# Kernel tuning notes

Measured on AMD Instinct MI355X. Metric: run time of the kernel, lower is better.

Reference implementation:

```python
import jax, jax.numpy as jnp
import numpy as np

D_MODEL = 1024
N_HEADS = 16
HEAD_DIM = D_MODEL // N_HEADS
ROPE_BASE = 10000.0


def _rope_cos_sin(seq_len, dtype):
    half = HEAD_DIM // 2
    theta = 1.0 / (ROPE_BASE ** (jnp.arange(half, dtype=jnp.float32) / half))
    freqs = jnp.arange(seq_len, dtype=jnp.float32)[:, None] * theta[None, :]  # [S, half]
    cos = jnp.repeat(jnp.cos(freqs), 2, axis=-1).astype(dtype)  # [S, HEAD_DIM]
    sin = jnp.repeat(jnp.sin(freqs), 2, axis=-1).astype(dtype)
    return cos[None, None, :, :], sin[None, None, :, :]


def _rotate_half(x):
    x_even = x[..., ::2]
    x_odd = x[..., 1::2]
    return jnp.stack((-x_odd, x_even), axis=-1).reshape(x.shape)


def setup_inputs() -> dict:
    key = jax.random.key(0)
    k1, k2, k3, k4, k5 = jax.random.split(key, 5)
    bsz, seq_len = 4, 2048
    s = 1.0 / np.sqrt(D_MODEL)
    return {
        "x": jax.random.normal(k1, (bsz, seq_len, D_MODEL), dtype=jnp.float32),
        "W_qkv": jax.random.uniform(k2, (3 * D_MODEL, D_MODEL), minval=-s, maxval=s, dtype=jnp.float32),
        "b_qkv": jax.random.uniform(k3, (3 * D_MODEL,), minval=-s, maxval=s, dtype=jnp.float32),
        "W_out": jax.random.uniform(k4, (D_MODEL, D_MODEL), minval=-s, maxval=s, dtype=jnp.float32),
        "b_out": jax.random.uniform(k5, (D_MODEL,), minval=-s, maxval=s, dtype=jnp.float32),
    }


def reference(x, W_qkv, b_qkv, W_out, b_out):
    bsz, seq_len, _ = x.shape
    qkv = x @ W_qkv.T + b_qkv  # [B, S, 3*D]
    qkv = qkv.reshape(bsz, seq_len, 3, N_HEADS, HEAD_DIM)
    q = jnp.transpose(qkv[:, :, 0], (0, 2, 1, 3))  # [B, H, S, Dh]
    k = jnp.transpose(qkv[:, :, 1], (0, 2, 1, 3))
    v = jnp.transpose(qkv[:, :, 2], (0, 2, 1, 3))
    cos, sin = _rope_cos_sin(seq_len, x.dtype)
    q = q * cos + _rotate_half(q) * sin
    k = k * cos + _rotate_half(k) * sin
    attn = jnp.einsum("bhqd,bhkd->bhqk", q, k) / jnp.sqrt(jnp.asarray(HEAD_DIM, x.dtype))
    attn = jax.nn.softmax(attn, axis=-1)
    out = jnp.einsum("bhqk,bhkd->bhqd", attn, v)  # [B, H, S, Dh]
    out = jnp.transpose(out, (0, 2, 1, 3)).reshape(bsz, seq_len, D_MODEL)
    return out @ W_out.T + b_out
```

## Files before the change

### kernel.cpp

```cpp
#include <hip/hip_runtime.h>
#include <math.h>

typedef unsigned int u32;
typedef unsigned short u16;
typedef short bf16x8 __attribute__((ext_vector_type(8)));
typedef u32 u32x4 __attribute__((ext_vector_type(4)));
typedef float f32x4 __attribute__((ext_vector_type(4)));

#define SEQ 2048
#define NH 16
#define HD 64
#define DM 1024

#define QSCALE 0.1803368801111204f

static __device__ __forceinline__ u16 f2bf(float f) {
  u32 u = __builtin_bit_cast(u32, f);
  u32 r = (u + 0x7FFFu + ((u >> 16) & 1u)) >> 16;
  return (u16)r;
}

#define GLDS16(gsrc, ldst)                                                        \
  __builtin_amdgcn_global_load_lds(                                               \
      (const __attribute__((address_space(1))) void*)(gsrc),                      \
      (__attribute__((address_space(3))) void*)(ldst), 16, 0, 0)

static __device__ __forceinline__ int swz64(int r, int c) {
  return (r * 64 + c) ^ ((r & 7) * 8);
}

static __device__ __forceinline__ void swz_grid(int nx, int& bx, int& by) {
  int lid = blockIdx.y * nx + blockIdx.x;
  int nwg = nx * (int)gridDim.y;
  int chunk = nwg >> 3;
  int s = (lid & 7) * chunk + (lid >> 3);
  bx = s % nx;
  by = s / nx;
}

__global__ void cast_bf16_kernel(const float* __restrict__ src, u16* __restrict__ dst, int n) {
  int i = (blockIdx.x * blockDim.x + threadIdx.x) * 4;
  if (i >= n) return;
  float4 v = *reinterpret_cast<const float4*>(src + i);
  ushort4 o;
  o.x = f2bf(v.x); o.y = f2bf(v.y); o.z = f2bf(v.z); o.w = f2bf(v.w);
  *reinterpret_cast<ushort4*>(dst + i) = o;
}

__global__ void rope_table_kernel(float* __restrict__ ct, float* __restrict__ st) {
  int t = blockIdx.x * blockDim.x + threadIdx.x;
  int s = t >> 5, i = t & 31;
  double theta_d = pow(10000.0, -(double)i / 32.0);
  float th = (float)theta_d;
  float fr = (float)s * th;
  ct[t] = (float)cos((double)fr);
  st[t] = (float)sin((double)fr);
}

template <int EPI>
__global__ __launch_bounds__(256, 3) void gemm128(
    const u16* __restrict__ A, const u16* __restrict__ Bw,
    const float* __restrict__ bias,
    u16* __restrict__ Qo, u16* __restrict__ Ko, u16* __restrict__ Vo,
    const float* __restrict__ ct, const float* __restrict__ st,
    float* __restrict__ Co) {
  __shared__ u16 As[128 * 64];
  __shared__ u16 Bs[128 * 64];
  const int tid = threadIdx.x;
  const int lane = tid & 63;
  const int w = tid >> 6;
  const int wm = w >> 1, wn = w & 1;
  int bx, by;
  swz_grid(gridDim.x, bx, by);
  const int m0 = by * 128;
  const int n0 = (EPI == 2 ? 2048 : 0) + bx * 128;

  f32x4 acc[4][4];
#pragma unroll
  for (int i = 0; i < 4; i++)
#pragma unroll
    for (int j = 0; j < 4; j++) acc[i][j] = (f32x4){0.f, 0.f, 0.f, 0.f};

  for (int kt = 0; kt < 1024 / 64; ++kt) {
    const int k0 = kt * 64;
    __syncthreads();
#pragma unroll
    for (int c = 0; c < 4; ++c) {
      int e = ((c * 4 + w) * 64 + lane) * 8;
      int row = e >> 6, col = e & 63;
      GLDS16(A + (size_t)(m0 + row) * 1024 + k0 + col, &As[e]);
      GLDS16(Bw + (size_t)(n0 + row) * 1024 + k0 + col, &Bs[e]);
    }
    asm volatile("s_waitcnt vmcnt(0)" ::: "memory");
    __syncthreads();

    bf16x8 af[4][2], bfr[4][2];
#pragma unroll
    for (int i = 0; i < 4; i++) {
      int r = wm * 64 + i * 16 + (lane & 15);
#pragma unroll
      for (int kk = 0; kk < 2; kk++) {
        int kc = kk * 32 + (lane >> 4) * 8;
        af[i][kk] = *reinterpret_cast<const bf16x8*>(&As[r * 64 + kc]);
      }
    }
#pragma unroll
    for (int j = 0; j < 4; j++) {
      int r = wn * 64 + j * 16 + (lane & 15);
#pragma unroll
      for (int kk = 0; kk < 2; kk++) {
        int kc = kk * 32 + (lane >> 4) * 8;
        bfr[j][kk] = *reinterpret_cast<const bf16x8*>(&Bs[r * 64 + kc]);
      }
    }
#pragma unroll
    for (int kk = 0; kk < 2; kk++)
#pragma unroll
      for (int i = 0; i < 4; i++)
#pragma unroll
        for (int j = 0; j < 4; j++) {
          if (EPI == 2)
            acc[i][j] = __builtin_amdgcn_mfma_f32_16x16x32_bf16(bfr[j][kk], af[i][kk], acc[i][j], 0, 0, 0);
          else
            acc[i][j] = __builtin_amdgcn_mfma_f32_16x16x32_bf16(af[i][kk], bfr[j][kk], acc[i][j], 0, 0, 0);
        }
  }

  if (EPI == 0) {
    const int which = n0 >> 10;
#pragma unroll
    for (int i = 0; i < 4; i++) {
#pragma unroll
      for (int j = 0; j < 4; j++) {
        int n = n0 + wn * 64 + j * 16 + (lane & 15);
        int mb = m0 + wm * 64 + i * 16 + (lane >> 4) * 4;
        float bi = bias[n];
        int d = n & 63;
        int h = (n >> 6) & 15;
        f32x4 v = acc[i][j];
#pragma unroll
        for (int r = 0; r < 4; r++) {
          int m = mb + r;
          int b = m >> 11, s = m & 2047;
          float vf = v[r] + bi;
          float pf = __shfl_xor(vf, 1, 64);
          float c = ct[s * 32 + (d >> 1)];
          float sn = st[s * 32 + (d >> 1)];
          float res = (d & 1) ? (vf * c + pf * sn) : (vf * c - pf * sn);
          if (which == 0) res *= QSCALE;
          u16 hv = f2bf(res);
          int bh = b * 16 + h;
          if (which == 0)
            Qo[((size_t)bh * 2048 + s) * 64 + d] = hv;
          else
            Ko[((size_t)bh * 2048 + s) * 64 + d] = hv;
        }
      }
    }
  } else if (EPI == 2) {
#pragma unroll
    for (int i = 0; i < 4; i++) {
#pragma unroll
      for (int j = 0; j < 4; j++) {
        int nb = n0 + wn * 64 + j * 16 + (lane >> 4) * 4;
        int m = m0 + wm * 64 + i * 16 + (lane & 15);
        int b = m >> 11, s = m & 2047;
#pragma unroll
        for (int r = 0; r < 4; r++) {
          int n = nb + r;
          int d = n & 63;
          int h = (n >> 6) & 15;
          float vf = acc[i][j][r] + bias[n];
          Vo[((size_t)(b * 16 + h) * 64 + d) * 2048 + s] = f2bf(vf);
        }
      }
    }
  } else {
#pragma unroll
    for (int i = 0; i < 4; i++) {
#pragma unroll
      for (int j = 0; j < 4; j++) {
        int n = n0 + wn * 64 + j * 16 + (lane & 15);
        int mb = m0 + wm * 64 + i * 16 + (lane >> 4) * 4;
        float bi = bias[n];
#pragma unroll
        for (int r = 0; r < 4; r++) {
          Co[(size_t)(mb + r) * 1024 + n] = acc[i][j][r] + bi;
        }
      }
    }
  }
}

__global__ __launch_bounds__(256) void attn_kernel(
    const u16* __restrict__ Q, const u16* __restrict__ Kb,
    const u16* __restrict__ Vt, u16* __restrict__ AO) {
  __shared__ u16 Ks[64 * 64];
  __shared__ u16 Vs[64 * 64];
  const int tid = threadIdx.x;
  const int lane = tid & 63;
  const int w = tid >> 6;
  const int bh = blockIdx.y;
  const int b = bh >> 4, h = bh & 15;
  const size_t base = (size_t)bh * SEQ * HD;
  const int q0 = blockIdx.x * 64 + w * 16;
  const int qcol = lane & 15;
  const int g = lane >> 4;

  bf16x8 qf[2];
#pragma unroll
  for (int kk = 0; kk < 2; kk++)
    qf[kk] = *reinterpret_cast<const bf16x8*>(Q + base + (size_t)(q0 + qcol) * 64 + kk * 32 + g * 8);

  f32x4 o[4];
#pragma unroll
  for (int dt = 0; dt < 4; dt++) o[dt] = (f32x4){0.f, 0.f, 0.f, 0.f};
  float mr = -1e30f, lr = 0.f;

  const int srcA = qcol | ((2 * (g & 1)) << 4);
  const int srcB = srcA + 16;
  const bool hi2 = (g & 2) != 0;

  for (int t = 0; t < SEQ / 64; ++t) {
    __syncthreads();
#pragma unroll
    for (int c = 0; c < 2; ++c) {
      int e = ((c * 4 + w) * 64 + lane) * 8;
      int se = e ^ ((lane >> 3) * 8);
      GLDS16(Kb + base + (size_t)t * 4096 + se, &Ks[e]);
      int dd = se >> 6, jj = se & 63;
      GLDS16(Vt + base + (size_t)dd * 2048 + t * 64 + jj, &Vs[e]);
    }
    asm volatile("s_waitcnt vmcnt(0)" ::: "memory");
    __syncthreads();

    f32x4 sc[4];
    __builtin_amdgcn_s_setprio(1);
#pragma unroll
    for (int jt = 0; jt < 4; jt++) {
      f32x4 a = (f32x4){0.f, 0.f, 0.f, 0.f};
#pragma unroll
      for (int kk = 0; kk < 2; kk++) {
        bf16x8 kf = *reinterpret_cast<const bf16x8*>(&Ks[swz64(jt * 16 + qcol, kk * 32 + g * 8)]);
        a = __builtin_amdgcn_mfma_f32_16x16x32_bf16(kf, qf[kk], a, 0, 0, 0);
      }
      sc[jt] = a;
    }
    __builtin_amdgcn_s_setprio(0);

    float mx = fmaxf(fmaxf(sc[0][0], sc[0][1]), fmaxf(sc[0][2], sc[0][3]));
#pragma unroll
    for (int jt = 1; jt < 4; jt++)
      mx = fmaxf(mx, fmaxf(fmaxf(sc[jt][0], sc[jt][1]), fmaxf(sc[jt][2], sc[jt][3])));
    mx = fmaxf(mx, __shfl_xor(mx, 16, 64));
    mx = fmaxf(mx, __shfl_xor(mx, 32, 64));

    if (__any(mx > mr + 11.0f)) {
      float nm = fmaxf(mr, mx);
      float fs = __builtin_amdgcn_exp2f(mr - nm);
      mr = nm;
      lr *= fs;
      float fsq[4];
#pragma unroll
      for (int r = 0; r < 4; r++) fsq[r] = __shfl(fs, g * 4 + r, 64);
#pragma unroll
      for (int dt = 0; dt < 4; dt++)
#pragma unroll
        for (int r = 0; r < 4; r++) o[dt][r] *= fsq[r];
    }

    float ps = 0.f;
#pragma unroll
    for (int jt = 0; jt < 4; jt++)
#pragma unroll
      for (int r = 0; r < 4; r++) {
        float p = __builtin_amdgcn_exp2f(sc[jt][r] - mr);
        sc[jt][r] = p;
        ps += p;
      }
    ps += __shfl_xor(ps, 16, 64);
    ps += __shfl_xor(ps, 32, 64);
    lr += ps;

    u32 pk[4][2];
#pragma unroll
    for (int jt = 0; jt < 4; jt++) {
      asm("v_cvt_pk_bf16_f32 %0, %1, %2" : "=v"(pk[jt][0]) : "v"(sc[jt][0]), "v"(sc[jt][1]));
      asm("v_cvt_pk_bf16_f32 %0, %1, %2" : "=v"(pk[jt][1]) : "v"(sc[jt][2]), "v"(sc[jt][3]));
    }

    __builtin_amdgcn_s_setprio(1);
#pragma unroll
    for (int kk = 0; kk < 2; kk++) {
      u32x4 pav;
#pragma unroll
      for (int pidx = 0; pidx < 4; pidx++) {
        int src = (pidx & 2) ? srcB : srcA;
        u32 ta = __shfl(pk[2 * kk][pidx & 1], src, 64);
        u32 tb = __shfl(pk[2 * kk + 1][pidx & 1], src, 64);
        pav[pidx] = hi2 ? tb : ta;
      }
      bf16x8 pa = __builtin_bit_cast(bf16x8, pav);
#pragma unroll
      for (int dt = 0; dt < 4; dt++) {
        bf16x8 vf = *reinterpret_cast<const bf16x8*>(&Vs[swz64(dt * 16 + qcol, kk * 32 + g * 8)]);
        o[dt] = __builtin_amdgcn_mfma_f32_16x16x32_bf16(pa, vf, o[dt], 0, 0, 0);
      }
    }
    __builtin_amdgcn_s_setprio(0);
  }

  float lrq[4];
#pragma unroll
  for (int r = 0; r < 4; r++) lrq[r] = __shfl(lr, g * 4 + r, 64);
#pragma unroll
  for (int dt = 0; dt < 4; dt++)
#pragma unroll
    for (int r = 0; r < 4; r++) {
      int srow = q0 + g * 4 + r;
      AO[((size_t)(b * 2048 + srow)) * 1024 + h * 64 + dt * 16 + qcol] = f2bf(o[dt][r] / lrq[r]);
    }
}

extern "C" void kernel_launch(void* const* d_in, const int* in_sizes, int n_in,
                              void* d_out, int out_size, void* d_ws, size_t ws_size,
                              hipStream_t stream) {
  const float* x = (const float*)d_in[0];
  const float* Wqkv = (const float*)d_in[1];
  const float* bqkv = (const float*)d_in[2];
  const float* Wout = (const float*)d_in[3];
  const float* bout = (const float*)d_in[4];
  float* out = (float*)d_out;

  char* p = (char*)d_ws;
  float* ct = (float*)p; p += (size_t)65536 * 4;
  float* st = (float*)p; p += (size_t)65536 * 4;
  u16* Xb  = (u16*)p; p += (size_t)8388608 * 2;
  u16* Wqb = (u16*)p; p += (size_t)3145728 * 2;
  u16* Wob = (u16*)p; p += (size_t)1048576 * 2;
  u16* Qw  = (u16*)p; p += (size_t)8388608 * 2;
  u16* Kw  = (u16*)p; p += (size_t)8388608 * 2;
  u16* Vw  = (u16*)p; p += (size_t)8388608 * 2;
  u16* AO  = (u16*)p; p += (size_t)8388608 * 2;

  cast_bf16_kernel<<<8192, 256, 0, stream>>>(x, Xb, 8388608);
  cast_bf16_kernel<<<3072, 256, 0, stream>>>(Wqkv, Wqb, 3145728);
  cast_bf16_kernel<<<1024, 256, 0, stream>>>(Wout, Wob, 1048576);
  rope_table_kernel<<<256, 256, 0, stream>>>(ct, st);

  gemm128<0><<<dim3(16, 64), 256, 0, stream>>>(Xb, Wqb, bqkv, Qw, Kw, nullptr, ct, st, nullptr);
  gemm128<2><<<dim3(8, 64), 256, 0, stream>>>(Xb, Wqb, bqkv, nullptr, nullptr, Vw, nullptr, nullptr, nullptr);
  attn_kernel<<<dim3(32, 64), 256, 0, stream>>>(Qw, Kw, Vw, AO);
  gemm128<1><<<dim3(8, 64), 256, 0, stream>>>(AO, Wob, bout, nullptr, nullptr, nullptr, nullptr, nullptr, out);
}
```

Baseline: 348.0 us.

## Prefetch next K/V tile during softmax and vectorize RoPE epilogue stores

The attention loop now issues the next K tile and a double-buffered V tile right after the QK^T MFMAs, so global-to-LDS loads overlap the softmax and PV work instead of stalling at the top of each iteration. K stays single-buffered, guarded by a barrier placed after the QK reads. Separately, the QKV GEMM permutes its B-row loading so each lane holds both elements of a RoPE pair. The epilogue can then do the rotation without a cross-lane shuffle and write packed 32-bit bf16 pairs with a float2 bias load. The risks are more LDS use and subtle barrier ordering correctness.

```diff
diff --git a/kernel.cpp b/kernel.cpp
--- a/kernel.cpp
+++ b/kernel.cpp
@@ -89,7 +89,8 @@
       int e = ((c * 4 + w) * 64 + lane) * 8;
       int row = e >> 6, col = e & 63;
       GLDS16(A + (size_t)(m0 + row) * 1024 + k0 + col, &As[e]);
-      GLDS16(Bw + (size_t)(n0 + row) * 1024 + k0 + col, &Bs[e]);
+      int srow = (EPI == 0) ? (32 * (row >> 5) + 2 * (row & 15) + ((row >> 4) & 1)) : row;
+      GLDS16(Bw + (size_t)(n0 + srow) * 1024 + k0 + col, &Bs[e]);
     }
     asm volatile("s_waitcnt vmcnt(0)" ::: "memory");
     __syncthreads();
@@ -128,32 +129,30 @@
 
   if (EPI == 0) {
     const int which = n0 >> 10;
+    const int q = lane & 15;
 #pragma unroll
     for (int i = 0; i < 4; i++) {
-#pragma unroll
-      for (int j = 0; j < 4; j++) {
-        int n = n0 + wn * 64 + j * 16 + (lane & 15);
-        int mb = m0 + wm * 64 + i * 16 + (lane >> 4) * 4;
-        float bi = bias[n];
-        int d = n & 63;
-        int h = (n >> 6) & 15;
-        f32x4 v = acc[i][j];
+      int mb = m0 + wm * 64 + i * 16 + (lane >> 4) * 4;
+#pragma unroll
+      for (int t = 0; t < 2; t++) {
+        int n_e = n0 + wn * 64 + 32 * t + 2 * q;
+        int d_e = (wn * 64 + 32 * t + 2 * q) & 63;
+        int h = (n_e >> 6) & 15;
+        float2 bi = *reinterpret_cast<const float2*>(&bias[n_e]);
 #pragma unroll
         for (int r = 0; r < 4; r++) {
           int m = mb + r;
           int b = m >> 11, s = m & 2047;
-          float vf = v[r] + bi;
-          float pf = __shfl_xor(vf, 1, 64);
-          float c = ct[s * 32 + (d >> 1)];
-          float sn = st[s * 32 + (d >> 1)];
-          float res = (d & 1) ? (vf * c + pf * sn) : (vf * c - pf * sn);
-          if (which == 0) res *= QSCALE;
-          u16 hv = f2bf(res);
-          int bh = b * 16 + h;
-          if (which == 0)
-            Qo[((size_t)bh * 2048 + s) * 64 + d] = hv;
-          else
-            Ko[((size_t)bh * 2048 + s) * 64 + d] = hv;
+          float ve = acc[i][2 * t][r] + bi.x;
+          float vo = acc[i][2 * t + 1][r] + bi.y;
+          float c = ct[s * 32 + 16 * t + q];
+          float sn = st[s * 32 + 16 * t + q];
+          float re = ve * c - vo * sn;
+          float ro = vo * c + ve * sn;
+          if (which == 0) { re *= QSCALE; ro *= QSCALE; }
+          u32 pkd = (u32)f2bf(re) | ((u32)f2bf(ro) << 16);
+          u16* dst = (which == 0) ? Qo : Ko;
+          *reinterpret_cast<u32*>(&dst[((size_t)(b * 16 + h) * 2048 + s) * 64 + d_e]) = pkd;
         }
       }
     }
@@ -196,7 +195,7 @@
     const u16* __restrict__ Q, const u16* __restrict__ Kb,
     const u16* __restrict__ Vt, u16* __restrict__ AO) {
   __shared__ u16 Ks[64 * 64];
-  __shared__ u16 Vs[64 * 64];
+  __shared__ u16 Vs[2][64 * 64];
   const int tid = threadIdx.x;
   const int lane = tid & 63;
   const int w = tid >> 6;
@@ -221,19 +220,30 @@
   const int srcB = srcA + 16;
   const bool hi2 = (g & 2) != 0;
 
+  const int e0 = ((0 * 4 + w) * 64 + lane) * 8;
+  const int e1 = ((1 * 4 + w) * 64 + lane) * 8;
+  const int se0 = e0 ^ ((lane >> 3) * 8);
+  const int se1 = e1 ^ ((lane >> 3) * 8);
+
+#define STAGE_K(t)                                                \
+  do {                                                            \
+    GLDS16(Kb + base + (size_t)(t) * 4096 + se0, &Ks[e0]);        \
+    GLDS16(Kb + base + (size_t)(t) * 4096 + se1, &Ks[e1]);        \
+  } while (0)
+#define STAGE_V(t, pb)                                                          \
+  do {                                                                          \
+    GLDS16(Vt + base + (size_t)(se0 >> 6) * 2048 + (t) * 64 + (se0 & 63),       \
+           &Vs[pb][e0]);                                                        \
+    GLDS16(Vt + base + (size_t)(se1 >> 6) * 2048 + (t) * 64 + (se1 & 63),       \
+           &Vs[pb][e1]);                                                        \
+  } while (0)
+
+  STAGE_K(0);
+  STAGE_V(0, 0);
+  asm volatile("s_waitcnt vmcnt(0)" ::: "memory");
+  __builtin_amdgcn_s_barrier();
+
   for (int t = 0; t < SEQ / 64; ++t) {
-    __syncthreads();
-#pragma unroll
-    for (int c = 0; c < 2; ++c) {
-      int e = ((c * 4 + w) * 64 + lane) * 8;
-      int se = e ^ ((lane >> 3) * 8);
-      GLDS16(Kb + base + (size_t)t * 4096 + se, &Ks[e]);
-      int dd = se >> 6, jj = se & 63;
-      GLDS16(Vt + base + (size_t)dd * 2048 + t * 64 + jj, &Vs[e]);
-    }
-    asm volatile("s_waitcnt vmcnt(0)" ::: "memory");
-    __syncthreads();
-
     f32x4 sc[4];
     __builtin_amdgcn_s_setprio(1);
 #pragma unroll
@@ -247,6 +257,12 @@
       sc[jt] = a;
     }
     __builtin_amdgcn_s_setprio(0);
+
+    __builtin_amdgcn_s_barrier();
+    if (t + 1 < SEQ / 64) {
+      STAGE_K(t + 1);
+      STAGE_V(t + 1, (t + 1) & 1);
+    }
 
     float mx = fmaxf(fmaxf(sc[0][0], sc[0][1]), fmaxf(sc[0][2], sc[0][3]));
 #pragma unroll
@@ -289,6 +305,7 @@
       asm("v_cvt_pk_bf16_f32 %0, %1, %2" : "=v"(pk[jt][1]) : "v"(sc[jt][2]), "v"(sc[jt][3]));
     }
 
+    const u16* vsb = Vs[t & 1];
     __builtin_amdgcn_s_setprio(1);
 #pragma unroll
     for (int kk = 0; kk < 2; kk++) {
@@ -303,12 +320,17 @@
       bf16x8 pa = __builtin_bit_cast(bf16x8, pav);
 #pragma unroll
       for (int dt = 0; dt < 4; dt++) {
-        bf16x8 vf = *reinterpret_cast<const bf16x8*>(&Vs[swz64(dt * 16 + qcol, kk * 32 + g * 8)]);
+        bf16x8 vf = *reinterpret_cast<const bf16x8*>(&vsb[swz64(dt * 16 + qcol, kk * 32 + g * 8)]);
         o[dt] = __builtin_amdgcn_mfma_f32_16x16x32_bf16(pa, vf, o[dt], 0, 0, 0);
       }
     }
     __builtin_amdgcn_s_setprio(0);
+
+    asm volatile("s_waitcnt vmcnt(0)" ::: "memory");
+    __builtin_amdgcn_s_barrier();
   }
+#undef STAGE_K
+#undef STAGE_V
 
   float lrq[4];
 #pragma unroll
```

Measured after the change: 344.4 us. Within noise of the previous version (-1.0%).
